# Optimization experiments

Hardware: AMD Instinct MI355X
Metric: run time of the kernel (lower is better)

## Reference

```python
import jax, jax.numpy as jnp
import numpy as np
from jax import lax

AGG_HOPS = 3
RANK_K = 10
NEG = -1e9


def _aggregate(embs, agg_w, agg_b, W_last, b_last):
    # GIKT-style multi-hop mean aggregation: embs[j] has shape [B, n1..nj, D]
    embs = list(embs)
    for i in range(AGG_HOPS):
        for j in range(AGG_HOPS - i):
            s = jnp.mean(embs[j + 1], axis=-2) + embs[j]
            embs[j] = jnp.tanh(s @ agg_w[j].T + agg_b[j])
    return jnp.tanh(embs[0] @ W_last.T + b_last)


def _hops(nodes0, tabA, tabB):
    # alternating bipartite neighbor expansion: [B] -> [B,n] -> [B,n,n] -> ...
    lst = [nodes0]
    for i in range(AGG_HOPS):
        tab = tabA if i % 2 == 0 else tabB
        lst.append(tab[lst[-1]])
    return lst


def _forward(user, question, response, mask, q_neighbors, s_neighbors, u_neighbors,
             q_neighbors_2, qs_index, emb_question, emb_question_2, emb_skill,
             emb_user, emb_response, w1_q, w2_q, W_ih, W_hh, b_ih, b_hh,
             agg_w, agg_b, W_agg_last, b_agg_last, W_query, b_query, W_key, b_key,
             W_w, b_w, W_fusion, b_fusion):
    B, T = question.shape
    D = emb_question.shape[1]
    emb_q_all = emb_question[question]  # [B,T,D], used for recap similarity
    wA, wB = W_w[0, :D], W_w[0, D:]     # MLP_W(cat(Q,K)) = Q@wA + K@wB + b

    def predict(qs_concat, states, svalid):
        ql = (qs_concat @ W_query.T + b_query) @ wA          # [B,Lq]
        kl = (states @ W_key.T + b_key) @ wB                 # [B,Ls]
        logit = ql[:, :, None] + kl[:, None, :] + b_w[0]     # [B,Lq,Ls]
        logit = jnp.where(svalid[:, None, :], logit, NEG)
        Lq, Ls = logit.shape[1], logit.shape[2]
        alpha = jax.nn.softmax(logit.reshape(B, -1), axis=1).reshape(B, Lq, Ls)
        g = jnp.einsum('bqd,bsd->bqs', qs_concat, states)
        return jax.nn.sigmoid(jnp.sum(alpha * g, axis=(1, 2)))

    def step(carry, t):
        h, c, sh = carry
        q_t, u_t, r_t = question[:, t], user[:, t], response[:, t]
        m = (mask[:, t] == 1)[:, None]  # [B,1]
        # question-skill GNN branch
        embs_q = [(emb_question if i % 2 == 0 else emb_skill)[n]
                  for i, n in enumerate(_hops(q_t, q_neighbors, s_neighbors))]
        e1 = jnp.where(m, _aggregate(embs_q, agg_w, agg_b, W_agg_last, b_agg_last),
                       emb_question[q_t])
        # user-question GNN branch
        embs_u = [(emb_user if i % 2 == 0 else emb_question_2)[n]
                  for i, n in enumerate(_hops(u_t, u_neighbors, q_neighbors_2))]
        e2 = jnp.where(m, _aggregate(embs_u, agg_w, agg_b, W_agg_last, b_agg_last),
                       emb_question_2[q_t])
        e_hat = w1_q * e1 + w2_q * e2
        e_t = jax.nn.relu(jnp.concatenate([e_hat, emb_response[r_t]], axis=1)
                          @ W_fusion.T + b_fusion)
        # masked LSTMCell (torch gate order i,f,g,o); dropout in eval mode
        gates = e_t @ W_ih.T + b_ih + h @ W_hh.T + b_hh
        gi, gf, gg, go = jnp.split(gates, 4, axis=1)
        c2 = jax.nn.sigmoid(gf) * c + jax.nn.sigmoid(gi) * jnp.tanh(gg)
        h2 = jax.nn.sigmoid(go) * jnp.tanh(c2)
        h = jnp.where(m, h2, h)
        c = jnp.where(m, c2, c)
        sh = lax.dynamic_update_slice(sh, h[:, None, :], (0, t, 0))
        # next question + its related skills
        q_next = question[:, t + 1]
        emb_qn = emb_question[q_next]
        qs_concat = jnp.concatenate([emb_qn[:, None, :], emb_skill[qs_index[q_next]]], axis=1)
        # soft recap: top-k past states by (detached) question similarity
        scores = lax.stop_gradient(jnp.einsum('btd,bd->bt', emb_q_all, emb_qn))
        valid_t = jnp.arange(T) < t
        scores = jnp.where(valid_t[None, :], scores, NEG)
        _, idx = lax.top_k(scores, RANK_K)                    # [B,K]
        sel = jnp.take_along_axis(sh, idx[:, :, None], axis=1)  # [B,K,D]
        svalid = jnp.concatenate([jnp.ones((B, 1), bool), valid_t[idx]], axis=1)
        states = jnp.concatenate([h[:, None, :], sel], axis=1)  # [B,1+K,D]
        y = predict(qs_concat, states, svalid)
        return (h, c, sh), y

    h0 = jnp.zeros((B, D), jnp.float32)
    sh0 = jnp.zeros((B, T, D), jnp.float32)
    _, ys = lax.scan(step, (h0, h0, sh0), jnp.arange(T - 1))
    return jnp.concatenate([jnp.full((B, 1), 0.5, jnp.float32), ys.T], axis=1)


def setup_inputs() -> dict:
    B, T, D = 32, 50, 100
    NQ, NS, NU = 20000, 500, 10000
    NBR, SPQ = 6, 4
    key = jax.random.key(0)
    ks = iter(jax.random.split(key, 48))
    nrm = lambda shape, sc: jax.random.normal(next(ks), shape, jnp.float32) * sc
    ri = lambda shape, hi: jax.random.randint(next(ks), shape, 0, hi, jnp.int32)
    s = 1.0 / float(np.sqrt(D))
    return {
        'user': ri((B, T), NU), 'question': ri((B, T), NQ),
        'response': ri((B, T), 2), 'mask': ri((B, T), 2),
        'q_neighbors': ri((NQ, NBR), NS), 's_neighbors': ri((NS, NBR), NQ),
        'u_neighbors': ri((NU, NBR), NQ), 'q_neighbors_2': ri((NQ, NBR), NU),
        'qs_index': ri((NQ, SPQ), NS),
        'emb_question': nrm((NQ, D), 0.1), 'emb_question_2': nrm((NQ, D), 0.1),
        'emb_skill': nrm((NS, D), 0.1), 'emb_user': nrm((NU, D), 0.1),
        'emb_response': nrm((2, D), 0.1),
        'w1_q': jnp.float32(0.5), 'w2_q': jnp.float32(0.5),
        'W_ih': nrm((4 * D, D), s), 'W_hh': nrm((4 * D, D), s),
        'b_ih': jnp.zeros((4 * D,), jnp.float32), 'b_hh': jnp.zeros((4 * D,), jnp.float32),
        'agg_w': nrm((3, D, D), s), 'agg_b': jnp.zeros((3, D), jnp.float32),
        'W_agg_last': nrm((D, D), s), 'b_agg_last': jnp.zeros((D,), jnp.float32),
        'W_query': nrm((D, D), s), 'b_query': jnp.zeros((D,), jnp.float32),
        'W_key': nrm((D, D), s), 'b_key': jnp.zeros((D,), jnp.float32),
        'W_w': nrm((1, 2 * D), s), 'b_w': jnp.zeros((1,), jnp.float32),
        'W_fusion': nrm((D, 2 * D), s), 'b_fusion': jnp.zeros((D,), jnp.float32),
    }


def reference(user, question, response, mask, q_neighbors, s_neighbors, u_neighbors,
              q_neighbors_2, qs_index, emb_question, emb_question_2, emb_skill,
              emb_user, emb_response, w1_q, w2_q, W_ih, W_hh, b_ih, b_hh,
              agg_w, agg_b, W_agg_last, b_agg_last, W_query, b_query, W_key, b_key,
              W_w, b_w, W_fusion, b_fusion):
    return _forward(user, question, response, mask, q_neighbors, s_neighbors,
                    u_neighbors, q_neighbors_2, qs_index, emb_question,
                    emb_question_2, emb_skill, emb_user, emb_response, w1_q, w2_q,
                    W_ih, W_hh, b_ih, b_hh, agg_w, agg_b, W_agg_last, b_agg_last,
                    W_query, b_query, W_key, b_key, W_w, b_w, W_fusion, b_fusion)
```

## Files before the change

kernel.cpp:

```cpp
#include <hip/hip_runtime.h>
#include <hip/hip_bf16.h>

#define BSZ 32
#define TT 50
#define TS 49
#define PH 101

#define OFF_GPRE  0u
#define OFF_QL    627200u
#define OFF_IDX   639744u
#define OFF_NV    655424u
#define OFF_QSC   656992u
#define OFF_E1    1440992u
#define OFF_E2    1597792u

#define RLF(v,l) __uint_as_float(__builtin_amdgcn_readlane(__float_as_uint(v), (l)))

__device__ __forceinline__ float tanh_fast(float x) {
    float e = __expf(2.f * x);
    return 1.f - __fdividef(2.f, e + 1.f);
}
__device__ __forceinline__ float sigm_fast(float x) {
    return __fdividef(1.f, 1.f + __expf(-x));
}
__device__ __forceinline__ float dot4(float4 a, float4 b) {
    return a.x*b.x + a.y*b.y + a.z*b.z + a.w*b.w;
}

__global__ __launch_bounds__(256, 2) void kagg(
    const int* __restrict__ user, const int* __restrict__ question, const int* __restrict__ mask,
    const int* __restrict__ qnbr, const int* __restrict__ snbr,
    const int* __restrict__ unbr, const int* __restrict__ qnbr2,
    const float* __restrict__ embQ, const float* __restrict__ embQ2, const float* __restrict__ embS,
    const float* __restrict__ embU,
    const float* __restrict__ aggw, const float* __restrict__ aggb,
    const float* __restrict__ wlast, const float* __restrict__ blast,
    float* __restrict__ WS)
{
    int bid = blockIdx.x;
    int tid = threadIdx.x;

    int pair = bid >> 1, which = bid & 1;
    int b = pair / TS, t = pair - b*TS;
    int mm = mask[b*TT + t];
    float* outE = WS + (which ? OFF_E2 : OFF_E1) + (size_t)pair*100;

    if (mm != 1) {
        int q_t = question[b*TT + t];
        const float4* src = (const float4*)((which ? embQ2 : embQ) + (size_t)q_t*100);
        if (tid < 25) ((float4*)outE)[tid] = src[tid];
        return;
    }

    int root = which ? user[b*TT + t] : question[b*TT + t];
    const int*   tabA = which ? unbr  : qnbr;
    const int*   tabB = which ? qnbr2 : snbr;
    const float4* eE = (const float4*)(which ? embU  : embQ);
    const float4* eO = (const float4*)(which ? embQ2 : embS);

    __shared__ __align__(16) float b2in[36*108];
    __shared__ __align__(16) float x1[6*108];
    __shared__ float s2v1b[600];
    __shared__ float v1a[600];
    __shared__ __align__(16) float x0[104], v0a[104], v0b[104];
    __shared__ int n1[8], n2[36], n3[216];

    if (tid < 6) n1[tid] = tabA[root*6 + tid];
    __syncthreads();
    if (tid < 36) n2[tid] = tabB[n1[tid/6]*6 + (tid % 6)];
    __syncthreads();
    if (tid < 216) n3[tid] = tabA[n2[tid/6]*6 + (tid % 6)];
    __syncthreads();
    for (int i4 = tid; i4 < 900; i4 += 256) {
        int v = i4 / 25, j = i4 - v*25;
        float4 a = eE[(size_t)n2[v]*25 + j];
        float4 s = make_float4(0.f, 0.f, 0.f, 0.f);
        const int* p = n3 + v*6;
        #pragma unroll
        for (int c = 0; c < 6; ++c) {
            float4 o = eO[(size_t)p[c]*25 + j];
            s.x += o.x; s.y += o.y; s.z += o.z; s.w += o.w;
        }
        float4 r = make_float4(a.x + s.x*(1.f/6.f), a.y + s.y*(1.f/6.f),
                               a.z + s.z*(1.f/6.f), a.w + s.w*(1.f/6.f));
        *(float4*)(b2in + v*108 + 4*j) = r;
    }
    for (int i4 = tid; i4 < 150; i4 += 256) {
        int a = i4 / 25, j = i4 - a*25;
        float4 base = eO[(size_t)n1[a]*25 + j];
        float4 s = make_float4(0.f, 0.f, 0.f, 0.f);
        #pragma unroll
        for (int c = 0; c < 6; ++c) {
            float4 o = eE[(size_t)n2[a*6 + c]*25 + j];
            s.x += o.x; s.y += o.y; s.z += o.z; s.w += o.w;
        }
        float4 r = make_float4(base.x + s.x*(1.f/6.f), base.y + s.y*(1.f/6.f),
                               base.z + s.z*(1.f/6.f), base.w + s.w*(1.f/6.f));
        *(float4*)(x1 + a*108 + 4*j) = r;
    }
    if (tid >= 160 && tid < 185) {
        int j = tid - 160;
        float4 base = eE[(size_t)root*25 + j];
        float4 s = make_float4(0.f, 0.f, 0.f, 0.f);
        #pragma unroll
        for (int a = 0; a < 6; ++a) {
            float4 o = eO[(size_t)n1[a]*25 + j];
            s.x += o.x; s.y += o.y; s.z += o.z; s.w += o.w;
        }
        float4 r = make_float4(base.x + s.x*(1.f/6.f), base.y + s.y*(1.f/6.f),
                               base.z + s.z*(1.f/6.f), base.w + s.w*(1.f/6.f));
        *(float4*)(x0 + 4*j) = r;
    }
    __syncthreads();
    if (tid < 150) {
        int dblk = tid / 6, a = tid - dblk*6, d0 = dblk*4;
        const float* wp = aggw + 20000 + d0*100;
        const float* xb = b2in + a*648;
        float acc[4][6];
        #pragma unroll
        for (int r = 0; r < 4; ++r)
            #pragma unroll
            for (int c = 0; c < 6; ++c) acc[r][c] = 0.f;
        #pragma unroll
        for (int j = 0; j < 25; ++j) {
            float4 r0 = *(const float4*)(wp + 4*j);
            float4 r1 = *(const float4*)(wp + 100 + 4*j);
            float4 r2 = *(const float4*)(wp + 200 + 4*j);
            float4 r3 = *(const float4*)(wp + 300 + 4*j);
            #pragma unroll
            for (int c = 0; c < 6; ++c) {
                float4 x = *(const float4*)(xb + c*108 + 4*j);
                acc[0][c] += dot4(r0, x);
                acc[1][c] += dot4(r1, x);
                acc[2][c] += dot4(r2, x);
                acc[3][c] += dot4(r3, x);
            }
        }
        #pragma unroll
        for (int r = 0; r < 4; ++r) {
            float bia = aggb[200 + d0 + r];
            float o = 0.f;
            #pragma unroll
            for (int c = 0; c < 6; ++c) o += tanh_fast(bia + acc[r][c]);
            s2v1b[a*100 + d0 + r] = o;
        }
    } else if (tid >= 160 && tid < 210) {
        int d0 = (tid - 160)*2;
        const float* wp = aggw + 10000 + d0*100;
        float a0[6], a1[6];
        #pragma unroll
        for (int c = 0; c < 6; ++c) { a0[c] = 0.f; a1[c] = 0.f; }
        #pragma unroll
        for (int j = 0; j < 25; ++j) {
            float4 r0 = *(const float4*)(wp + 4*j);
            float4 r1 = *(const float4*)(wp + 100 + 4*j);
            #pragma unroll
            for (int c = 0; c < 6; ++c) {
                float4 x = *(const float4*)(x1 + c*108 + 4*j);
                a0[c] += dot4(r0, x);
                a1[c] += dot4(r1, x);
            }
        }
        #pragma unroll
        for (int c = 0; c < 6; ++c) {
            v1a[c*100 + d0]     = tanh_fast(aggb[100 + d0] + a0[c]);
            v1a[c*100 + d0 + 1] = tanh_fast(aggb[100 + d0 + 1] + a1[c]);
        }
    } else if (tid >= 216 && tid < 241) {
        int d0 = (tid - 216)*4;
        const float* wp = aggw + d0*100;
        float a0 = 0.f, a1 = 0.f, a2 = 0.f, a3 = 0.f;
        #pragma unroll
        for (int j = 0; j < 25; ++j) {
            float4 x = *(const float4*)(x0 + 4*j);
            a0 += dot4(*(const float4*)(wp + 4*j), x);
            a1 += dot4(*(const float4*)(wp + 100 + 4*j), x);
            a2 += dot4(*(const float4*)(wp + 200 + 4*j), x);
            a3 += dot4(*(const float4*)(wp + 300 + 4*j), x);
        }
        v0a[d0]   = tanh_fast(aggb[d0] + a0);
        v0a[d0+1] = tanh_fast(aggb[d0+1] + a1);
        v0a[d0+2] = tanh_fast(aggb[d0+2] + a2);
        v0a[d0+3] = tanh_fast(aggb[d0+3] + a3);
    }
    __syncthreads();
    for (int e = tid; e < 600; e += 256) {
        int a = e / 100, d = e - a*100;
        x1[a*108 + d] = v1a[a*100 + d] + s2v1b[a*100 + d]*(1.f/6.f);
    }
    if (tid >= 128 && tid < 228) {
        int d = tid - 128;
        float s = 0.f;
        #pragma unroll
        for (int a = 0; a < 6; ++a) s += v1a[a*100 + d];
        x0[d] = v0a[d] + s*(1.f/6.f);
    }
    __syncthreads();
    if (tid < 50) {
        int d0 = tid*2;
        const float* wp = aggw + 10000 + d0*100;
        float a0[6], a1[6];
        #pragma unroll
        for (int c = 0; c < 6; ++c) { a0[c] = 0.f; a1[c] = 0.f; }
        #pragma unroll
        for (int j = 0; j < 25; ++j) {
            float4 r0 = *(const float4*)(wp + 4*j);
            float4 r1 = *(const float4*)(wp + 100 + 4*j);
            #pragma unroll
            for (int c = 0; c < 6; ++c) {
                float4 x = *(const float4*)(x1 + c*108 + 4*j);
                a0[c] += dot4(r0, x);
                a1[c] += dot4(r1, x);
            }
        }
        #pragma unroll
        for (int c = 0; c < 6; ++c) {
            s2v1b[c*100 + d0]     = tanh_fast(aggb[100 + d0] + a0[c]);
            s2v1b[c*100 + d0 + 1] = tanh_fast(aggb[100 + d0 + 1] + a1[c]);
        }
    } else if (tid >= 64 && tid < 89) {
        int d0 = (tid - 64)*4;
        const float* wp = aggw + d0*100;
        float a0 = 0.f, a1 = 0.f, a2 = 0.f, a3 = 0.f;
        #pragma unroll
        for (int j = 0; j < 25; ++j) {
            float4 x = *(const float4*)(x0 + 4*j);
            a0 += dot4(*(const float4*)(wp + 4*j), x);
            a1 += dot4(*(const float4*)(wp + 100 + 4*j), x);
            a2 += dot4(*(const float4*)(wp + 200 + 4*j), x);
            a3 += dot4(*(const float4*)(wp + 300 + 4*j), x);
        }
        v0b[d0]   = tanh_fast(aggb[d0] + a0);
        v0b[d0+1] = tanh_fast(aggb[d0+1] + a1);
        v0b[d0+2] = tanh_fast(aggb[d0+2] + a2);
        v0b[d0+3] = tanh_fast(aggb[d0+3] + a3);
    }
    __syncthreads();
    if (tid < 100) {
        float s = 0.f;
        #pragma unroll
        for (int a = 0; a < 6; ++a) s += s2v1b[a*100 + tid];
        x0[tid] = v0b[tid] + s*(1.f/6.f);
    }
    __syncthreads();
    if (tid < 25) {
        int d0 = tid*4;
        const float* wp = aggw + d0*100;
        float a0 = 0.f, a1 = 0.f, a2 = 0.f, a3 = 0.f;
        #pragma unroll
        for (int j = 0; j < 25; ++j) {
            float4 x = *(const float4*)(x0 + 4*j);
            a0 += dot4(*(const float4*)(wp + 4*j), x);
            a1 += dot4(*(const float4*)(wp + 100 + 4*j), x);
            a2 += dot4(*(const float4*)(wp + 200 + 4*j), x);
            a3 += dot4(*(const float4*)(wp + 300 + 4*j), x);
        }
        v0a[d0]   = tanh_fast(aggb[d0] + a0);
        v0a[d0+1] = tanh_fast(aggb[d0+1] + a1);
        v0a[d0+2] = tanh_fast(aggb[d0+2] + a2);
        v0a[d0+3] = tanh_fast(aggb[d0+3] + a3);
    }
    __syncthreads();
    if (tid < 25) {
        int d0 = tid*4;
        const float* wp = wlast + d0*100;
        float a0 = 0.f, a1 = 0.f, a2 = 0.f, a3 = 0.f;
        #pragma unroll
        for (int j = 0; j < 25; ++j) {
            float4 x = *(const float4*)(v0a + 4*j);
            a0 += dot4(*(const float4*)(wp + 4*j), x);
            a1 += dot4(*(const float4*)(wp + 100 + 4*j), x);
            a2 += dot4(*(const float4*)(wp + 200 + 4*j), x);
            a3 += dot4(*(const float4*)(wp + 300 + 4*j), x);
        }
        float4 r = make_float4(tanh_fast(blast[d0] + a0), tanh_fast(blast[d0+1] + a1),
                               tanh_fast(blast[d0+2] + a2), tanh_fast(blast[d0+3] + a3));
        *(float4*)(outE + d0) = r;
    }
}

__global__ __launch_bounds__(256, 2) void kfuse(
    const int* __restrict__ question, const int* __restrict__ response,
    const int* __restrict__ qsidx,
    const float* __restrict__ embQ, const float* __restrict__ embS, const float* __restrict__ embR,
    const float* __restrict__ w1p, const float* __restrict__ w2p,
    const float* __restrict__ wfus, const float* __restrict__ bfus,
    const float* __restrict__ wih, const float* __restrict__ bih, const float* __restrict__ bhh,
    const float* __restrict__ wq, const float* __restrict__ bq, const float* __restrict__ ww,
    float* __restrict__ WS)
{
    int bid = blockIdx.x;
    int b = bid / TS, t = bid - b*TS;
    int tid = threadIdx.x;
    size_t bt = (size_t)b*TS + t;

    __shared__ __align__(16) float sEIN[200], sET[112], sEQN[104], sQSCm[500];
    __shared__ float sWW[104], sVQ[104], sScore[52], sCq[1];

    int r_t = response[b*TT + t];
    int qn  = question[b*TT + t + 1];
    if (tid < 100) {
        sEIN[tid] = w1p[0]*WS[OFF_E1 + bt*100 + tid] + w2p[0]*WS[OFF_E2 + bt*100 + tid];
    } else if (tid < 200) {
        sEIN[tid] = embR[r_t*100 + (tid - 100)];
        if (tid < 150) {
            int d = tid - 100;
            sEQN[d]      = embQ[(size_t)qn*100 + d];
            sEQN[d + 50] = embQ[(size_t)qn*100 + d + 50];
        }
    } else {
        for (int i = tid - 200; i < 100; i += 56) sWW[i] = ww[i];
    }
    __syncthreads();
    if (tid < 160) {
        int slot = tid >> 4, k0 = tid & 15;
        #pragma unroll
        for (int rp = 0; rp < 10; ++rp) {
            int row = rp*10 + slot;
            const float* wr = wfus + row*200;
            float acc = 0.f;
            #pragma unroll
            for (int m = 0; m < 4; ++m) {
                int f4i = k0 + 16*m;
                if (f4i < 50)
                    acc += dot4(*(const float4*)(wr + 4*f4i), *(const float4*)(sEIN + 4*f4i));
            }
            acc += __shfl_xor(acc, 1); acc += __shfl_xor(acc, 2);
            acc += __shfl_xor(acc, 4); acc += __shfl_xor(acc, 8);
            if (k0 == 0) sET[row] = fmaxf(acc + bfus[row], 0.f);
        }
    } else {
        for (int k = tid - 160; k < 100; k += 96) {
            float a = 0.f;
            for (int d = 0; d < 100; ++d) a += sWW[d] * wq[d*100 + k];
            sVQ[k] = a;
        }
        if (tid == 255) {
            float a = 0.f;
            for (int d = 0; d < 100; ++d) a += bq[d] * sWW[d];
            sCq[0] = a;
        }
    }
    __syncthreads();
    {
        int slot = tid >> 4, k0 = tid & 15;
        #pragma unroll 4
        for (int rp = 0; rp < 25; ++rp) {
            int row = rp*16 + slot;
            const float* wr = wih + row*100;
            float acc = 0.f;
            #pragma unroll
            for (int m = 0; m < 2; ++m) {
                int f4i = k0 + 16*m;
                if (f4i < 25)
                    acc += dot4(*(const float4*)(wr + 4*f4i), *(const float4*)(sET + 4*f4i));
            }
            acc += __shfl_xor(acc, 1); acc += __shfl_xor(acc, 2);
            acc += __shfl_xor(acc, 4); acc += __shfl_xor(acc, 8);
            if (k0 == 0) WS[OFF_GPRE + bt*400 + row] = acc + bih[row] + bhh[row];
        }
    }
    if (tid < 125) {
        int q = tid / 25, j = tid - q*25;
        float4 val = (q == 0) ? *(const float4*)(sEQN + 4*j)
                              : ((const float4*)embS)[(size_t)qsidx[qn*4 + (q-1)]*25 + j];
        *(float4*)(sQSCm + q*100 + 4*j) = val;
        *(float4*)(WS + OFF_QSC + bt*500 + q*100 + 4*j) = val;
    } else if (tid >= 128 && tid < 128 + TS) {
        int tp = tid - 128;
        if (tp < t) {
            int qq = question[b*TT + tp];
            const float* er = embQ + (size_t)qq*100;
            float acc = 0.f;
            #pragma unroll
            for (int k = 0; k < 25; ++k)
                acc += dot4(*(const float4*)(er + 4*k), *(const float4*)(sEQN + 4*k));
            sScore[tp] = acc;
        }
    }
    __syncthreads();
    if (tid < 80) {
        int q = tid >> 4, kk = tid & 15;
        float acc = 0.f;
        #pragma unroll
        for (int j = 0; j < 7; ++j) {
            int k = kk + 16*j;
            if (k < 100) acc = fmaf(sQSCm[q*100 + k], sVQ[k], acc);
        }
        acc += __shfl_xor(acc, 1); acc += __shfl_xor(acc, 2);
        acc += __shfl_xor(acc, 4); acc += __shfl_xor(acc, 8);
        if (kk == 0) WS[OFF_QL + bt*8 + q] = acc + sCq[0];
    }
    if (tid >= 128 && tid < 192) {
        int lane = tid - 128;
        int nv = t < 10 ? t : 10;
        int* idxp = (int*)(WS + OFF_IDX) + bt*10;
        if (lane == 0) ((int*)(WS + OFF_NV))[bt] = nv;
        float v = (lane < t) ? sScore[lane] : -3.0e38f;
        int myidx = lane;
        int taken = 0;
        for (int p = 0; p < 10; ++p) {
            float vv = taken ? -3.0e38f : v;
            int ii = myidx;
            #pragma unroll
            for (int m = 1; m < 64; m <<= 1) {
                float v2 = __shfl_xor(vv, m);
                int   i2 = __shfl_xor(ii, m);
                if (v2 > vv || (v2 == vv && i2 < ii)) { vv = v2; ii = i2; }
            }
            if (p < nv) {
                if (lane == 0) idxp[p] = ii;
                if (myidx == ii) taken = 1;
            } else if (lane == 0) idxp[p] = 0;
        }
    }
}

__global__ __launch_bounds__(576) void kseq(
    const int* __restrict__ mask, const float* __restrict__ whh,
    const float* __restrict__ wk, const float* __restrict__ bk,
    const float* __restrict__ ww, const float* __restrict__ bwp,
    const float* __restrict__ WS, float* __restrict__ out)
{
    int b = blockIdx.x, tid = threadIdx.x, lane = tid & 63;
    __shared__ float sQSCall[TS*500];
    __shared__ float sSH[TS*PH + 3];
    __shared__ float sQLall[TS*8];
    __shared__ int   sIdxAll[TS*10];
    __shared__ int   sNvAll[TS];
    __shared__ int   sMask[TT];
    __shared__ float sH[104], sC[104], sG[400], sVKl[104];
    __shared__ float sKL2[2][12], sGv2[2][64];
    __shared__ float sCk[1];

    size_t b0 = (size_t)b*TS;
    int g = tid - 64;
    bool isGate = (g >= 0 && g < 400);

    float4 wv[25];
    if (isGate) {
        #pragma unroll
        for (int j = 0; j < 25; ++j) wv[j] = *(const float4*)(whh + g*100 + 4*j);
    }
    float gpre = isGate ? WS[OFF_GPRE + b0*400 + g] : 0.f;

    for (int i = tid; i < TS*500; i += 576) sQSCall[i] = WS[OFF_QSC + b0*500 + i];
    for (int i = tid; i < TS*8;   i += 576) sQLall[i]  = WS[OFF_QL + b0*8 + i];
    for (int i = tid; i < TS*10;  i += 576) sIdxAll[i] = ((const int*)(WS + OFF_IDX))[b0*10 + i];
    for (int i = tid; i < TS;     i += 576) sNvAll[i]  = ((const int*)(WS + OFF_NV))[b0 + i];
    if (tid < TT) sMask[tid] = mask[b*TT + tid];
    if (tid < 104) { sH[tid] = 0.f; sC[tid] = 0.f; }
    if (tid >= 104 && tid < 204) {
        int k = tid - 104;
        float a = 0.f;
        for (int d = 0; d < 100; ++d) a += ww[100 + d] * wk[d*100 + k];
        sVKl[k] = a;
    }
    if (tid == 204) {
        float a = 0.f;
        for (int d = 0; d < 100; ++d) a += bk[d] * ww[100 + d];
        sCk[0] = a;
    }
    if (tid == 205) out[b*TT] = 0.5f;
    float bw = bwp[0];
    __syncthreads();
    float ck = sCk[0];

    for (int t = 0; t < TS; ++t) {
        int par = t & 1;
        if (isGate) {
            float hA = sH[lane];
            float hB = sH[64 + (lane % 36)];
            float gpre_nx = 0.f;
            if (t + 1 < TS) gpre_nx = WS[OFF_GPRE + (b0 + t + 1)*400 + g];
            float a0 = 0.f, a1 = 0.f, a2 = 0.f, a3 = 0.f;
            #pragma unroll
            for (int j = 0; j < 25; ++j) {
                const int kb = 4*j;
                float h0, h1, h2, h3;
                if (kb < 64) {
                    h0 = RLF(hA, kb);   h1 = RLF(hA, kb+1);
                    h2 = RLF(hA, kb+2); h3 = RLF(hA, kb+3);
                } else {
                    h0 = RLF(hB, kb-64); h1 = RLF(hB, kb-63);
                    h2 = RLF(hB, kb-62); h3 = RLF(hB, kb-61);
                }
                a0 = fmaf(h0, wv[j].x, a0);
                a1 = fmaf(h1, wv[j].y, a1);
                a2 = fmaf(h2, wv[j].z, a2);
                a3 = fmaf(h3, wv[j].w, a3);
            }
            sG[g] = (a0 + a1) + (a2 + a3) + gpre;
            gpre = gpre_nx;
        } else if (tid >= 512) {
            int nv = sNvAll[t];
            if (lane < 60) {
                bool isKL = lane < 10;
                int s = isKL ? (lane + 1) : (((lane - 10) % 10) + 1);
                int q = isKL ? 0 : ((lane - 10) / 10);
                if (s <= nv) {
                    const float* st = sSH + sIdxAll[t*10 + s - 1]*PH;
                    const float* xp = isKL ? sVKl : (sQSCall + t*500 + q*100);
                    float c0 = 0.f, c1 = 0.f, c2 = 0.f, c3 = 0.f;
                    #pragma unroll
                    for (int k = 0; k < 100; k += 4) {
                        c0 = fmaf(st[k],   xp[k],   c0);
                        c1 = fmaf(st[k+1], xp[k+1], c1);
                        c2 = fmaf(st[k+2], xp[k+2], c2);
                        c3 = fmaf(st[k+3], xp[k+3], c3);
                    }
                    float acc = (c0 + c1) + (c2 + c3);
                    if (isKL) sKL2[par][s] = acc + ck;
                    else      sGv2[par][q*12 + s] = acc;
                }
            }
        } else if (tid < 64 && t > 0) {
            int tau = t - 1, par2 = tau & 1;
            int nv = sNvAll[tau];
            int dd = lane >> 3, k0 = lane & 7;
            if (dd < 6) {
                const float* xp = (dd == 0) ? sVKl : (sQSCall + tau*500 + (dd-1)*100);
                float acc = 0.f;
                #pragma unroll
                for (int jj = 0; jj < 13; ++jj) {
                    int k = k0 + 8*jj;
                    if (k < 100) acc = fmaf(sH[k], xp[k], acc);
                }
                acc += __shfl_xor(acc, 1); acc += __shfl_xor(acc, 2); acc += __shfl_xor(acc, 4);
                if (k0 == 0) {
                    if (dd == 0) sKL2[par2][0] = acc + ck;
                    else         sGv2[par2][(dd-1)*12] = acc;
                }
            }
            int q = lane / 11, s = lane - q*11;
            bool valid = (lane < 55) && (s <= nv);
            float lg = valid ? (sQLall[tau*8 + q] + sKL2[par2][s] + bw) : 0.f;
            float e  = valid ? __expf(lg) : 0.f;
            float gv = valid ? sGv2[par2][q*12 + s] : 0.f;
            float se = e, sg = e*gv;
            #pragma unroll
            for (int m = 1; m < 64; m <<= 1) { se += __shfl_xor(se, m); sg += __shfl_xor(sg, m); }
            if (lane == 0) out[b*TT + tau + 1] = __fdividef(1.f, 1.f + __expf(-__fdividef(sg, se)));
        }
        __syncthreads();
        if (g >= 0 && g < 100) {
            float gi = sG[g], gf = sG[100+g], gg = sG[200+g], go = sG[300+g];
            float c2 = sigm_fast(gf)*sC[g] + sigm_fast(gi)*tanh_fast(gg);
            float h2 = sigm_fast(go)*tanh_fast(c2);
            if (sMask[t] == 1) { sH[g] = h2; sC[g] = c2; }
            sSH[t*PH + g] = sH[g];
        }
        __syncthreads();
    }
    if (tid < 64) {
        int tau = TS - 1, par2 = tau & 1;
        int nv = sNvAll[tau];
        int dd = lane >> 3, k0 = lane & 7;
        if (dd < 6) {
            const float* xp = (dd == 0) ? sVKl : (sQSCall + tau*500 + (dd-1)*100);
            float acc = 0.f;
            #pragma unroll
            for (int jj = 0; jj < 13; ++jj) {
                int k = k0 + 8*jj;
                if (k < 100) acc = fmaf(sH[k], xp[k], acc);
            }
            acc += __shfl_xor(acc, 1); acc += __shfl_xor(acc, 2); acc += __shfl_xor(acc, 4);
            if (k0 == 0) {
                if (dd == 0) sKL2[par2][0] = acc + ck;
                else         sGv2[par2][(dd-1)*12] = acc;
            }
        }
        int q = lane / 11, s = lane - q*11;
        bool valid = (lane < 55) && (s <= nv);
        float lg = valid ? (sQLall[tau*8 + q] + sKL2[par2][s] + bw) : 0.f;
        float e  = valid ? __expf(lg) : 0.f;
        float gv = valid ? sGv2[par2][q*12 + s] : 0.f;
        float se = e, sg = e*gv;
        #pragma unroll
        for (int m = 1; m < 64; m <<= 1) { se += __shfl_xor(se, m); sg += __shfl_xor(sg, m); }
        if (lane == 0) out[b*TT + tau + 1] = __fdividef(1.f, 1.f + __expf(-__fdividef(sg, se)));
    }
}

extern "C" void kernel_launch(void* const* d_in, const int* in_sizes, int n_in,
                              void* d_out, int out_size, void* d_ws, size_t ws_size,
                              hipStream_t stream) {
    const int* user      = (const int*)d_in[0];
    const int* question  = (const int*)d_in[1];
    const int* response  = (const int*)d_in[2];
    const int* mask      = (const int*)d_in[3];
    const int* qnbr      = (const int*)d_in[4];
    const int* snbr      = (const int*)d_in[5];
    const int* unbr      = (const int*)d_in[6];
    const int* qnbr2     = (const int*)d_in[7];
    const int* qsidx     = (const int*)d_in[8];
    const float* embQ    = (const float*)d_in[9];
    const float* embQ2   = (const float*)d_in[10];
    const float* embS    = (const float*)d_in[11];
    const float* embU    = (const float*)d_in[12];
    const float* embR    = (const float*)d_in[13];
    const float* w1      = (const float*)d_in[14];
    const float* w2      = (const float*)d_in[15];
    const float* wih     = (const float*)d_in[16];
    const float* whh     = (const float*)d_in[17];
    const float* bih     = (const float*)d_in[18];
    const float* bhh     = (const float*)d_in[19];
    const float* aggw    = (const float*)d_in[20];
    const float* aggb    = (const float*)d_in[21];
    const float* wlast   = (const float*)d_in[22];
    const float* blast   = (const float*)d_in[23];
    const float* wq      = (const float*)d_in[24];
    const float* bq      = (const float*)d_in[25];
    const float* wk      = (const float*)d_in[26];
    const float* bk      = (const float*)d_in[27];
    const float* ww      = (const float*)d_in[28];
    const float* bwp     = (const float*)d_in[29];
    const float* wfus    = (const float*)d_in[30];
    const float* bfus    = (const float*)d_in[31];
    float* WS = (float*)d_ws;
    float* out = (float*)d_out;

    hipLaunchKernelGGL(kagg, dim3(2*BSZ*TS), dim3(256), 0, stream,
                       user, question, mask, qnbr, snbr, unbr, qnbr2,
                       embQ, embQ2, embS, embU, aggw, aggb, wlast, blast, WS);
    hipLaunchKernelGGL(kfuse, dim3(BSZ*TS), dim3(256), 0, stream,
                       question, response, qsidx, embQ, embS, embR,
                       w1, w2, wfus, bfus, wih, bih, bhh, wq, bq, ww, WS);
    hipLaunchKernelGGL(kseq, dim3(BSZ), dim3(576), 0, stream,
                       mask, whh, wk, bk, ww, bwp, WS, out);
}
```

Before: 414.6 us.

## Fuse aggregation and fusion kernels into one 512-thread block per step

Merges the two GNN-aggregation blocks (question and user side) and the fusion/gate-precompute kernel into a single kernel, with 512 threads per (b,t): each 256-thread half runs one aggregation side into shared memory, then all threads do the fusion stage. The E1/E2 workspace round trip and one kernel launch go away, and the fusion work is spread over more threads. kseq's shared-memory loads are also switched to float4. In exchange, per-block shared memory and thread count grow, which may lower occupancy, and the masked steps leave half the block idle.

```diff
diff --git a/kernel.cpp b/kernel.cpp
--- a/kernel.cpp
+++ b/kernel.cpp
@@ -11,8 +11,6 @@
 #define OFF_IDX   639744u
 #define OFF_NV    655424u
 #define OFF_QSC   656992u
-#define OFF_E1    1440992u
-#define OFF_E2    1597792u
 
 #define RLF(v,l) __uint_as_float(__builtin_amdgcn_readlane(__float_as_uint(v), (l)))
 
@@ -27,262 +25,17 @@
     return a.x*b.x + a.y*b.y + a.z*b.z + a.w*b.w;
 }
 
-__global__ __launch_bounds__(256, 2) void kagg(
-    const int* __restrict__ user, const int* __restrict__ question, const int* __restrict__ mask,
+__global__ __launch_bounds__(512) void kab(
+    const int* __restrict__ user, const int* __restrict__ question,
+    const int* __restrict__ response, const int* __restrict__ mask,
     const int* __restrict__ qnbr, const int* __restrict__ snbr,
     const int* __restrict__ unbr, const int* __restrict__ qnbr2,
-    const float* __restrict__ embQ, const float* __restrict__ embQ2, const float* __restrict__ embS,
-    const float* __restrict__ embU,
+    const int* __restrict__ qsidx,
+    const float* __restrict__ embQ, const float* __restrict__ embQ2,
+    const float* __restrict__ embS, const float* __restrict__ embU,
+    const float* __restrict__ embR,
     const float* __restrict__ aggw, const float* __restrict__ aggb,
     const float* __restrict__ wlast, const float* __restrict__ blast,
-    float* __restrict__ WS)
-{
-    int bid = blockIdx.x;
-    int tid = threadIdx.x;
-
-    int pair = bid >> 1, which = bid & 1;
-    int b = pair / TS, t = pair - b*TS;
-    int mm = mask[b*TT + t];
-    float* outE = WS + (which ? OFF_E2 : OFF_E1) + (size_t)pair*100;
-
-    if (mm != 1) {
-        int q_t = question[b*TT + t];
-        const float4* src = (const float4*)((which ? embQ2 : embQ) + (size_t)q_t*100);
-        if (tid < 25) ((float4*)outE)[tid] = src[tid];
-        return;
-    }
-
-    int root = which ? user[b*TT + t] : question[b*TT + t];
-    const int*   tabA = which ? unbr  : qnbr;
-    const int*   tabB = which ? qnbr2 : snbr;
-    const float4* eE = (const float4*)(which ? embU  : embQ);
-    const float4* eO = (const float4*)(which ? embQ2 : embS);
-
-    __shared__ __align__(16) float b2in[36*108];
-    __shared__ __align__(16) float x1[6*108];
-    __shared__ float s2v1b[600];
-    __shared__ float v1a[600];
-    __shared__ __align__(16) float x0[104], v0a[104], v0b[104];
-    __shared__ int n1[8], n2[36], n3[216];
-
-    if (tid < 6) n1[tid] = tabA[root*6 + tid];
-    __syncthreads();
-    if (tid < 36) n2[tid] = tabB[n1[tid/6]*6 + (tid % 6)];
-    __syncthreads();
-    if (tid < 216) n3[tid] = tabA[n2[tid/6]*6 + (tid % 6)];
-    __syncthreads();
-    for (int i4 = tid; i4 < 900; i4 += 256) {
-        int v = i4 / 25, j = i4 - v*25;
-        float4 a = eE[(size_t)n2[v]*25 + j];
-        float4 s = make_float4(0.f, 0.f, 0.f, 0.f);
-        const int* p = n3 + v*6;
-        #pragma unroll
-        for (int c = 0; c < 6; ++c) {
-            float4 o = eO[(size_t)p[c]*25 + j];
-            s.x += o.x; s.y += o.y; s.z += o.z; s.w += o.w;
-        }
-        float4 r = make_float4(a.x + s.x*(1.f/6.f), a.y + s.y*(1.f/6.f),
-                               a.z + s.z*(1.f/6.f), a.w + s.w*(1.f/6.f));
-        *(float4*)(b2in + v*108 + 4*j) = r;
-    }
-    for (int i4 = tid; i4 < 150; i4 += 256) {
-        int a = i4 / 25, j = i4 - a*25;
-        float4 base = eO[(size_t)n1[a]*25 + j];
-        float4 s = make_float4(0.f, 0.f, 0.f, 0.f);
-        #pragma unroll
-        for (int c = 0; c < 6; ++c) {
-            float4 o = eE[(size_t)n2[a*6 + c]*25 + j];
-            s.x += o.x; s.y += o.y; s.z += o.z; s.w += o.w;
-        }
-        float4 r = make_float4(base.x + s.x*(1.f/6.f), base.y + s.y*(1.f/6.f),
-                               base.z + s.z*(1.f/6.f), base.w + s.w*(1.f/6.f));
-        *(float4*)(x1 + a*108 + 4*j) = r;
-    }
-    if (tid >= 160 && tid < 185) {
-        int j = tid - 160;
-        float4 base = eE[(size_t)root*25 + j];
-        float4 s = make_float4(0.f, 0.f, 0.f, 0.f);
-        #pragma unroll
-        for (int a = 0; a < 6; ++a) {
-            float4 o = eO[(size_t)n1[a]*25 + j];
-            s.x += o.x; s.y += o.y; s.z += o.z; s.w += o.w;
-        }
-        float4 r = make_float4(base.x + s.x*(1.f/6.f), base.y + s.y*(1.f/6.f),
-                               base.z + s.z*(1.f/6.f), base.w + s.w*(1.f/6.f));
-        *(float4*)(x0 + 4*j) = r;
-    }
-    __syncthreads();
-    if (tid < 150) {
-        int dblk = tid / 6, a = tid - dblk*6, d0 = dblk*4;
-        const float* wp = aggw + 20000 + d0*100;
-        const float* xb = b2in + a*648;
-        float acc[4][6];
-        #pragma unroll
-        for (int r = 0; r < 4; ++r)
-            #pragma unroll
-            for (int c = 0; c < 6; ++c) acc[r][c] = 0.f;
-        #pragma unroll
-        for (int j = 0; j < 25; ++j) {
-            float4 r0 = *(const float4*)(wp + 4*j);
-            float4 r1 = *(const float4*)(wp + 100 + 4*j);
-            float4 r2 = *(const float4*)(wp + 200 + 4*j);
-            float4 r3 = *(const float4*)(wp + 300 + 4*j);
-            #pragma unroll
-            for (int c = 0; c < 6; ++c) {
-                float4 x = *(const float4*)(xb + c*108 + 4*j);
-                acc[0][c] += dot4(r0, x);
-                acc[1][c] += dot4(r1, x);
-                acc[2][c] += dot4(r2, x);
-                acc[3][c] += dot4(r3, x);
-            }
-        }
-        #pragma unroll
-        for (int r = 0; r < 4; ++r) {
-            float bia = aggb[200 + d0 + r];
-            float o = 0.f;
-            #pragma unroll
-            for (int c = 0; c < 6; ++c) o += tanh_fast(bia + acc[r][c]);
-            s2v1b[a*100 + d0 + r] = o;
-        }
-    } else if (tid >= 160 && tid < 210) {
-        int d0 = (tid - 160)*2;
-        const float* wp = aggw + 10000 + d0*100;
-        float a0[6], a1[6];
-        #pragma unroll
-        for (int c = 0; c < 6; ++c) { a0[c] = 0.f; a1[c] = 0.f; }
-        #pragma unroll
-        for (int j = 0; j < 25; ++j) {
-            float4 r0 = *(const float4*)(wp + 4*j);
-            float4 r1 = *(const float4*)(wp + 100 + 4*j);
-            #pragma unroll
-            for (int c = 0; c < 6; ++c) {
-                float4 x = *(const float4*)(x1 + c*108 + 4*j);
-                a0[c] += dot4(r0, x);
-                a1[c] += dot4(r1, x);
-            }
-        }
-        #pragma unroll
-        for (int c = 0; c < 6; ++c) {
-            v1a[c*100 + d0]     = tanh_fast(aggb[100 + d0] + a0[c]);
-            v1a[c*100 + d0 + 1] = tanh_fast(aggb[100 + d0 + 1] + a1[c]);
-        }
-    } else if (tid >= 216 && tid < 241) {
-        int d0 = (tid - 216)*4;
-        const float* wp = aggw + d0*100;
-        float a0 = 0.f, a1 = 0.f, a2 = 0.f, a3 = 0.f;
-        #pragma unroll
-        for (int j = 0; j < 25; ++j) {
-            float4 x = *(const float4*)(x0 + 4*j);
-            a0 += dot4(*(const float4*)(wp + 4*j), x);
-            a1 += dot4(*(const float4*)(wp + 100 + 4*j), x);
-            a2 += dot4(*(const float4*)(wp + 200 + 4*j), x);
-            a3 += dot4(*(const float4*)(wp + 300 + 4*j), x);
-        }
-        v0a[d0]   = tanh_fast(aggb[d0] + a0);
-        v0a[d0+1] = tanh_fast(aggb[d0+1] + a1);
-        v0a[d0+2] = tanh_fast(aggb[d0+2] + a2);
-        v0a[d0+3] = tanh_fast(aggb[d0+3] + a3);
-    }
-    __syncthreads();
-    for (int e = tid; e < 600; e += 256) {
-        int a = e / 100, d = e - a*100;
-        x1[a*108 + d] = v1a[a*100 + d] + s2v1b[a*100 + d]*(1.f/6.f);
-    }
-    if (tid >= 128 && tid < 228) {
-        int d = tid - 128;
-        float s = 0.f;
-        #pragma unroll
-        for (int a = 0; a < 6; ++a) s += v1a[a*100 + d];
-        x0[d] = v0a[d] + s*(1.f/6.f);
-    }
-    __syncthreads();
-    if (tid < 50) {
-        int d0 = tid*2;
-        const float* wp = aggw + 10000 + d0*100;
-        float a0[6], a1[6];
-        #pragma unroll
-        for (int c = 0; c < 6; ++c) { a0[c] = 0.f; a1[c] = 0.f; }
-        #pragma unroll
-        for (int j = 0; j < 25; ++j) {
-            float4 r0 = *(const float4*)(wp + 4*j);
-            float4 r1 = *(const float4*)(wp + 100 + 4*j);
-            #pragma unroll
-            for (int c = 0; c < 6; ++c) {
-                float4 x = *(const float4*)(x1 + c*108 + 4*j);
-                a0[c] += dot4(r0, x);
-                a1[c] += dot4(r1, x);
-            }
-        }
-        #pragma unroll
-        for (int c = 0; c < 6; ++c) {
-            s2v1b[c*100 + d0]     = tanh_fast(aggb[100 + d0] + a0[c]);
-            s2v1b[c*100 + d0 + 1] = tanh_fast(aggb[100 + d0 + 1] + a1[c]);
-        }
-    } else if (tid >= 64 && tid < 89) {
-        int d0 = (tid - 64)*4;
-        const float* wp = aggw + d0*100;
-        float a0 = 0.f, a1 = 0.f, a2 = 0.f, a3 = 0.f;
-        #pragma unroll
-        for (int j = 0; j < 25; ++j) {
-            float4 x = *(const float4*)(x0 + 4*j);
-            a0 += dot4(*(const float4*)(wp + 4*j), x);
-            a1 += dot4(*(const float4*)(wp + 100 + 4*j), x);
-            a2 += dot4(*(const float4*)(wp + 200 + 4*j), x);
-            a3 += dot4(*(const float4*)(wp + 300 + 4*j), x);
-        }
-        v0b[d0]   = tanh_fast(aggb[d0] + a0);
-        v0b[d0+1] = tanh_fast(aggb[d0+1] + a1);
-        v0b[d0+2] = tanh_fast(aggb[d0+2] + a2);
-        v0b[d0+3] = tanh_fast(aggb[d0+3] + a3);
-    }
-    __syncthreads();
-    if (tid < 100) {
-        float s = 0.f;
-        #pragma unroll
-        for (int a = 0; a < 6; ++a) s += s2v1b[a*100 + tid];
-        x0[tid] = v0b[tid] + s*(1.f/6.f);
-    }
-    __syncthreads();
-    if (tid < 25) {
-        int d0 = tid*4;
-        const float* wp = aggw + d0*100;
-        float a0 = 0.f, a1 = 0.f, a2 = 0.f, a3 = 0.f;
-        #pragma unroll
-        for (int j = 0; j < 25; ++j) {
-            float4 x = *(const float4*)(x0 + 4*j);
-            a0 += dot4(*(const float4*)(wp + 4*j), x);
-            a1 += dot4(*(const float4*)(wp + 100 + 4*j), x);
-            a2 += dot4(*(const float4*)(wp + 200 + 4*j), x);
-            a3 += dot4(*(const float4*)(wp + 300 + 4*j), x);
-        }
-        v0a[d0]   = tanh_fast(aggb[d0] + a0);
-        v0a[d0+1] = tanh_fast(aggb[d0+1] + a1);
-        v0a[d0+2] = tanh_fast(aggb[d0+2] + a2);
-        v0a[d0+3] = tanh_fast(aggb[d0+3] + a3);
-    }
-    __syncthreads();
-    if (tid < 25) {
-        int d0 = tid*4;
-        const float* wp = wlast + d0*100;
-        float a0 = 0.f, a1 = 0.f, a2 = 0.f, a3 = 0.f;
-        #pragma unroll
-        for (int j = 0; j < 25; ++j) {
-            float4 x = *(const float4*)(v0a + 4*j);
-            a0 += dot4(*(const float4*)(wp + 4*j), x);
-            a1 += dot4(*(const float4*)(wp + 100 + 4*j), x);
-            a2 += dot4(*(const float4*)(wp + 200 + 4*j), x);
-            a3 += dot4(*(const float4*)(wp + 300 + 4*j), x);
-        }
-        float4 r = make_float4(tanh_fast(blast[d0] + a0), tanh_fast(blast[d0+1] + a1),
-                               tanh_fast(blast[d0+2] + a2), tanh_fast(blast[d0+3] + a3));
-        *(float4*)(outE + d0) = r;
-    }
-}
-
-__global__ __launch_bounds__(256, 2) void kfuse(
-    const int* __restrict__ question, const int* __restrict__ response,
-    const int* __restrict__ qsidx,
-    const float* __restrict__ embQ, const float* __restrict__ embS, const float* __restrict__ embR,
     const float* __restrict__ w1p, const float* __restrict__ w2p,
     const float* __restrict__ wfus, const float* __restrict__ bfus,
     const float* __restrict__ wih, const float* __restrict__ bih, const float* __restrict__ bhh,
@@ -292,24 +45,271 @@
     int bid = blockIdx.x;
     int b = bid / TS, t = bid - b*TS;
     int tid = threadIdx.x;
+    int side = tid >> 8, ltid = tid & 255;
     size_t bt = (size_t)b*TS + t;
 
+    __shared__ __align__(16) float POOL[2][6608];
+    __shared__ int nbuf[2][264];
+    __shared__ __align__(16) float sE1[104], sE2[104];
     __shared__ __align__(16) float sEIN[200], sET[112], sEQN[104], sQSCm[500];
     __shared__ float sWW[104], sVQ[104], sScore[52], sCq[1];
 
+    int mm  = mask[b*TT + t];
+    int q_t = question[b*TT + t];
     int r_t = response[b*TT + t];
     int qn  = question[b*TT + t + 1];
+
+    if (mm == 1) {
+        int root = side ? user[b*TT + t] : q_t;
+        const int*    tabA = side ? unbr  : qnbr;
+        const int*    tabB = side ? qnbr2 : snbr;
+        const float4* eE   = (const float4*)(side ? embU  : embQ);
+        const float4* eO   = (const float4*)(side ? embQ2 : embS);
+        float* P     = POOL[side];
+        float* b2in  = P;
+        float* x1    = P + 3888;
+        float* s2v1b = P + 4536;
+        float* v1a   = P + 5136;
+        float* x0    = P + 5736;
+        float* v0a   = P + 5840;
+        float* v0b   = P + 5944;
+        int* n1 = nbuf[side];
+        int* n2 = n1 + 8;
+        int* n3 = n1 + 48;
+        float* sEout = side ? sE2 : sE1;
+
+        if (ltid < 6) n1[ltid] = tabA[root*6 + ltid];
+        __syncthreads();
+        if (ltid < 36) n2[ltid] = tabB[n1[ltid/6]*6 + (ltid % 6)];
+        __syncthreads();
+        if (ltid < 216) n3[ltid] = tabA[n2[ltid/6]*6 + (ltid % 6)];
+        __syncthreads();
+        for (int i4 = ltid; i4 < 900; i4 += 256) {
+            int v = i4 / 25, j = i4 - v*25;
+            float4 a = eE[(size_t)n2[v]*25 + j];
+            float4 s = make_float4(0.f, 0.f, 0.f, 0.f);
+            const int* p = n3 + v*6;
+            #pragma unroll
+            for (int c = 0; c < 6; ++c) {
+                float4 o = eO[(size_t)p[c]*25 + j];
+                s.x += o.x; s.y += o.y; s.z += o.z; s.w += o.w;
+            }
+            float4 r = make_float4(a.x + s.x*(1.f/6.f), a.y + s.y*(1.f/6.f),
+                                   a.z + s.z*(1.f/6.f), a.w + s.w*(1.f/6.f));
+            *(float4*)(b2in + v*108 + 4*j) = r;
+        }
+        for (int i4 = ltid; i4 < 150; i4 += 256) {
+            int a = i4 / 25, j = i4 - a*25;
+            float4 base = eO[(size_t)n1[a]*25 + j];
+            float4 s = make_float4(0.f, 0.f, 0.f, 0.f);
+            #pragma unroll
+            for (int c = 0; c < 6; ++c) {
+                float4 o = eE[(size_t)n2[a*6 + c]*25 + j];
+                s.x += o.x; s.y += o.y; s.z += o.z; s.w += o.w;
+            }
+            float4 r = make_float4(base.x + s.x*(1.f/6.f), base.y + s.y*(1.f/6.f),
+                                   base.z + s.z*(1.f/6.f), base.w + s.w*(1.f/6.f));
+            *(float4*)(x1 + a*108 + 4*j) = r;
+        }
+        if (ltid >= 160 && ltid < 185) {
+            int j = ltid - 160;
+            float4 base = eE[(size_t)root*25 + j];
+            float4 s = make_float4(0.f, 0.f, 0.f, 0.f);
+            #pragma unroll
+            for (int a = 0; a < 6; ++a) {
+                float4 o = eO[(size_t)n1[a]*25 + j];
+                s.x += o.x; s.y += o.y; s.z += o.z; s.w += o.w;
+            }
+            float4 r = make_float4(base.x + s.x*(1.f/6.f), base.y + s.y*(1.f/6.f),
+                                   base.z + s.z*(1.f/6.f), base.w + s.w*(1.f/6.f));
+            *(float4*)(x0 + 4*j) = r;
+        }
+        __syncthreads();
+        if (ltid < 150) {
+            int dblk = ltid / 6, a = ltid - dblk*6, d0 = dblk*4;
+            const float* wp = aggw + 20000 + d0*100;
+            const float* xb = b2in + a*648;
+            float acc[4][6];
+            #pragma unroll
+            for (int r = 0; r < 4; ++r)
+                #pragma unroll
+                for (int c = 0; c < 6; ++c) acc[r][c] = 0.f;
+            #pragma unroll
+            for (int j = 0; j < 25; ++j) {
+                float4 r0 = *(const float4*)(wp + 4*j);
+                float4 r1 = *(const float4*)(wp + 100 + 4*j);
+                float4 r2 = *(const float4*)(wp + 200 + 4*j);
+                float4 r3 = *(const float4*)(wp + 300 + 4*j);
+                #pragma unroll
+                for (int c = 0; c < 6; ++c) {
+                    float4 x = *(const float4*)(xb + c*108 + 4*j);
+                    acc[0][c] += dot4(r0, x);
+                    acc[1][c] += dot4(r1, x);
+                    acc[2][c] += dot4(r2, x);
+                    acc[3][c] += dot4(r3, x);
+                }
+            }
+            #pragma unroll
+            for (int r = 0; r < 4; ++r) {
+                float bia = aggb[200 + d0 + r];
+                float o = 0.f;
+                #pragma unroll
+                for (int c = 0; c < 6; ++c) o += tanh_fast(bia + acc[r][c]);
+                s2v1b[a*100 + d0 + r] = o;
+            }
+        } else if (ltid >= 160 && ltid < 210) {
+            int d0 = (ltid - 160)*2;
+            const float* wp = aggw + 10000 + d0*100;
+            float a0[6], a1[6];
+            #pragma unroll
+            for (int c = 0; c < 6; ++c) { a0[c] = 0.f; a1[c] = 0.f; }
+            #pragma unroll
+            for (int j = 0; j < 25; ++j) {
+                float4 r0 = *(const float4*)(wp + 4*j);
+                float4 r1 = *(const float4*)(wp + 100 + 4*j);
+                #pragma unroll
+                for (int c = 0; c < 6; ++c) {
+                    float4 x = *(const float4*)(x1 + c*108 + 4*j);
+                    a0[c] += dot4(r0, x);
+                    a1[c] += dot4(r1, x);
+                }
+            }
+            #pragma unroll
+            for (int c = 0; c < 6; ++c) {
+                v1a[c*100 + d0]     = tanh_fast(aggb[100 + d0] + a0[c]);
+                v1a[c*100 + d0 + 1] = tanh_fast(aggb[100 + d0 + 1] + a1[c]);
+            }
+        } else if (ltid >= 216 && ltid < 241) {
+            int d0 = (ltid - 216)*4;
+            const float* wp = aggw + d0*100;
+            float a0 = 0.f, a1 = 0.f, a2 = 0.f, a3 = 0.f;
+            #pragma unroll
+            for (int j = 0; j < 25; ++j) {
+                float4 x = *(const float4*)(x0 + 4*j);
+                a0 += dot4(*(const float4*)(wp + 4*j), x);
+                a1 += dot4(*(const float4*)(wp + 100 + 4*j), x);
+                a2 += dot4(*(const float4*)(wp + 200 + 4*j), x);
+                a3 += dot4(*(const float4*)(wp + 300 + 4*j), x);
+            }
+            v0a[d0]   = tanh_fast(aggb[d0] + a0);
+            v0a[d0+1] = tanh_fast(aggb[d0+1] + a1);
+            v0a[d0+2] = tanh_fast(aggb[d0+2] + a2);
+            v0a[d0+3] = tanh_fast(aggb[d0+3] + a3);
+        }
+        __syncthreads();
+        for (int e = ltid; e < 600; e += 256) {
+            int a = e / 100, d = e - a*100;
+            x1[a*108 + d] = v1a[a*100 + d] + s2v1b[a*100 + d]*(1.f/6.f);
+        }
+        if (ltid >= 128 && ltid < 228) {
+            int d = ltid - 128;
+            float s = 0.f;
+            #pragma unroll
+            for (int a = 0; a < 6; ++a) s += v1a[a*100 + d];
+            x0[d] = v0a[d] + s*(1.f/6.f);
+        }
+        __syncthreads();
+        if (ltid < 50) {
+            int d0 = ltid*2;
+            const float* wp = aggw + 10000 + d0*100;
+            float a0[6], a1[6];
+            #pragma unroll
+            for (int c = 0; c < 6; ++c) { a0[c] = 0.f; a1[c] = 0.f; }
+            #pragma unroll
+            for (int j = 0; j < 25; ++j) {
+                float4 r0 = *(const float4*)(wp + 4*j);
+                float4 r1 = *(const float4*)(wp + 100 + 4*j);
+                #pragma unroll
+                for (int c = 0; c < 6; ++c) {
+                    float4 x = *(const float4*)(x1 + c*108 + 4*j);
+                    a0[c] += dot4(r0, x);
+                    a1[c] += dot4(r1, x);
+                }
+            }
+            #pragma unroll
+            for (int c = 0; c < 6; ++c) {
+                s2v1b[c*100 + d0]     = tanh_fast(aggb[100 + d0] + a0[c]);
+                s2v1b[c*100 + d0 + 1] = tanh_fast(aggb[100 + d0 + 1] + a1[c]);
+            }
+        } else if (ltid >= 64 && ltid < 89) {
+            int d0 = (ltid - 64)*4;
+            const float* wp = aggw + d0*100;
+            float a0 = 0.f, a1 = 0.f, a2 = 0.f, a3 = 0.f;
+            #pragma unroll
+            for (int j = 0; j < 25; ++j) {
+                float4 x = *(const float4*)(x0 + 4*j);
+                a0 += dot4(*(const float4*)(wp + 4*j), x);
+                a1 += dot4(*(const float4*)(wp + 100 + 4*j), x);
+                a2 += dot4(*(const float4*)(wp + 200 + 4*j), x);
+                a3 += dot4(*(const float4*)(wp + 300 + 4*j), x);
+            }
+            v0b[d0]   = tanh_fast(aggb[d0] + a0);
+            v0b[d0+1] = tanh_fast(aggb[d0+1] + a1);
+            v0b[d0+2] = tanh_fast(aggb[d0+2] + a2);
+            v0b[d0+3] = tanh_fast(aggb[d0+3] + a3);
+        }
+        __syncthreads();
+        if (ltid < 100) {
+            float s = 0.f;
+            #pragma unroll
+            for (int a = 0; a < 6; ++a) s += s2v1b[a*100 + ltid];
+            x0[ltid] = v0b[ltid] + s*(1.f/6.f);
+        }
+        __syncthreads();
+        if (ltid < 25) {
+            int d0 = ltid*4;
+            const float* wp = aggw + d0*100;
+            float a0 = 0.f, a1 = 0.f, a2 = 0.f, a3 = 0.f;
+            #pragma unroll
+            for (int j = 0; j < 25; ++j) {
+                float4 x = *(const float4*)(x0 + 4*j);
+                a0 += dot4(*(const float4*)(wp + 4*j), x);
+                a1 += dot4(*(const float4*)(wp + 100 + 4*j), x);
+                a2 += dot4(*(const float4*)(wp + 200 + 4*j), x);
+                a3 += dot4(*(const float4*)(wp + 300 + 4*j), x);
+            }
+            v0a[d0]   = tanh_fast(aggb[d0] + a0);
+            v0a[d0+1] = tanh_fast(aggb[d0+1] + a1);
+            v0a[d0+2] = tanh_fast(aggb[d0+2] + a2);
+            v0a[d0+3] = tanh_fast(aggb[d0+3] + a3);
+        }
+        __syncthreads();
+        if (ltid < 25) {
+            int d0 = ltid*4;
+            const float* wp = wlast + d0*100;
+            float a0 = 0.f, a1 = 0.f, a2 = 0.f, a3 = 0.f;
+            #pragma unroll
+            for (int j = 0; j < 25; ++j) {
+                float4 x = *(const float4*)(v0a + 4*j);
+                a0 += dot4(*(const float4*)(wp + 4*j), x);
+                a1 += dot4(*(const float4*)(wp + 100 + 4*j), x);
+                a2 += dot4(*(const float4*)(wp + 200 + 4*j), x);
+                a3 += dot4(*(const float4*)(wp + 300 + 4*j), x);
+            }
+            float4 r = make_float4(tanh_fast(blast[d0] + a0), tanh_fast(blast[d0+1] + a1),
+                                   tanh_fast(blast[d0+2] + a2), tanh_fast(blast[d0+3] + a3));
+            *(float4*)(sEout + d0) = r;
+        }
+    } else {
+        if (tid < 25)
+            ((float4*)sE1)[tid] = ((const float4*)embQ)[(size_t)q_t*25 + tid];
+        else if (tid >= 256 && tid < 281)
+            ((float4*)sE2)[tid - 256] = ((const float4*)embQ2)[(size_t)q_t*25 + (tid - 256)];
+    }
+    __syncthreads();
+
     if (tid < 100) {
-        sEIN[tid] = w1p[0]*WS[OFF_E1 + bt*100 + tid] + w2p[0]*WS[OFF_E2 + bt*100 + tid];
+        sEIN[tid] = w1p[0]*sE1[tid] + w2p[0]*sE2[tid];
     } else if (tid < 200) {
         sEIN[tid] = embR[r_t*100 + (tid - 100)];
-        if (tid < 150) {
-            int d = tid - 100;
-            sEQN[d]      = embQ[(size_t)qn*100 + d];
-            sEQN[d + 50] = embQ[(size_t)qn*100 + d + 50];
-        }
-    } else {
-        for (int i = tid - 200; i < 100; i += 56) sWW[i] = ww[i];
+    } else if (tid < 300) {
+        sEQN[tid - 200] = embQ[(size_t)qn*100 + (tid - 200)];
+    } else if (tid < 400) {
+        sWW[tid - 300] = ww[tid - 300];
+    } else if (tid < 500) {
+        int i = tid - 400, q = i/25 + 1, j = i - (q-1)*25;
+        float4 v = ((const float4*)embS)[(size_t)qsidx[qn*4 + (q-1)]*25 + j];
+        *(float4*)(sQSCm + q*100 + 4*j) = v;
     }
     __syncthreads();
     if (tid < 160) {
@@ -329,7 +329,7 @@
             acc += __shfl_xor(acc, 4); acc += __shfl_xor(acc, 8);
             if (k0 == 0) sET[row] = fmaxf(acc + bfus[row], 0.f);
         }
-    } else {
+    } else if (tid < 256) {
         for (int k = tid - 160; k < 100; k += 96) {
             float a = 0.f;
             for (int d = 0; d < 100; ++d) a += sWW[d] * wq[d*100 + k];
@@ -340,34 +340,8 @@
             for (int d = 0; d < 100; ++d) a += bq[d] * sWW[d];
             sCq[0] = a;
         }
-    }
-    __syncthreads();
-    {
-        int slot = tid >> 4, k0 = tid & 15;
-        #pragma unroll 4
-        for (int rp = 0; rp < 25; ++rp) {
-            int row = rp*16 + slot;
-            const float* wr = wih + row*100;
-            float acc = 0.f;
-            #pragma unroll
-            for (int m = 0; m < 2; ++m) {
-                int f4i = k0 + 16*m;
-                if (f4i < 25)
-                    acc += dot4(*(const float4*)(wr + 4*f4i), *(const float4*)(sET + 4*f4i));
-            }
-            acc += __shfl_xor(acc, 1); acc += __shfl_xor(acc, 2);
-            acc += __shfl_xor(acc, 4); acc += __shfl_xor(acc, 8);
-            if (k0 == 0) WS[OFF_GPRE + bt*400 + row] = acc + bih[row] + bhh[row];
-        }
-    }
-    if (tid < 125) {
-        int q = tid / 25, j = tid - q*25;
-        float4 val = (q == 0) ? *(const float4*)(sEQN + 4*j)
-                              : ((const float4*)embS)[(size_t)qsidx[qn*4 + (q-1)]*25 + j];
-        *(float4*)(sQSCm + q*100 + 4*j) = val;
-        *(float4*)(WS + OFF_QSC + bt*500 + q*100 + 4*j) = val;
-    } else if (tid >= 128 && tid < 128 + TS) {
-        int tp = tid - 128;
+    } else if (tid < 256 + TS) {
+        int tp = tid - 256;
         if (tp < t) {
             int qq = question[b*TT + tp];
             const float* er = embQ + (size_t)qq*100;
@@ -377,10 +351,37 @@
                 acc += dot4(*(const float4*)(er + 4*k), *(const float4*)(sEQN + 4*k));
             sScore[tp] = acc;
         }
+    } else if (tid >= 320 && tid < 445) {
+        int i = tid - 320, q = i / 25, j = i - q*25;
+        float4 v = (q == 0) ? *(const float4*)(sEQN + 4*j)
+                            : *(const float4*)(sQSCm + q*100 + 4*j);
+        if (q == 0) *(float4*)(sQSCm + 4*j) = v;
+        *(float4*)(WS + OFF_QSC + bt*500 + q*100 + 4*j) = v;
     }
     __syncthreads();
-    if (tid < 80) {
-        int q = tid >> 4, kk = tid & 15;
+    {
+        int slot = tid >> 4, k0 = tid & 15;
+        #pragma unroll
+        for (int rp = 0; rp < 13; ++rp) {
+            int row = rp*32 + slot;
+            float acc = 0.f;
+            if (row < 400) {
+                const float* wr = wih + row*100;
+                #pragma unroll
+                for (int m = 0; m < 2; ++m) {
+                    int f4i = k0 + 16*m;
+                    if (f4i < 25)
+                        acc += dot4(*(const float4*)(wr + 4*f4i), *(const float4*)(sET + 4*f4i));
+                }
+            }
+            acc += __shfl_xor(acc, 1); acc += __shfl_xor(acc, 2);
+            acc += __shfl_xor(acc, 4); acc += __shfl_xor(acc, 8);
+            if (k0 == 0 && row < 400)
+                WS[OFF_GPRE + bt*400 + row] = acc + bih[row] + bhh[row];
+        }
+    }
+    if (tid >= 384 && tid < 464) {
+        int q = (tid - 384) >> 4, kk = tid & 15;
         float acc = 0.f;
         #pragma unroll
         for (int j = 0; j < 7; ++j) {
@@ -391,8 +392,8 @@
         acc += __shfl_xor(acc, 4); acc += __shfl_xor(acc, 8);
         if (kk == 0) WS[OFF_QL + bt*8 + q] = acc + sCq[0];
     }
-    if (tid >= 128 && tid < 192) {
-        int lane = tid - 128;
+    if (tid >= 320 && tid < 384) {
+        int lane = tid - 320;
         int nv = t < 10 ? t : 10;
         int* idxp = (int*)(WS + OFF_IDX) + bt*10;
         if (lane == 0) ((int*)(WS + OFF_NV))[bt] = nv;
@@ -423,9 +424,9 @@
     const float* __restrict__ WS, float* __restrict__ out)
 {
     int b = blockIdx.x, tid = threadIdx.x, lane = tid & 63;
-    __shared__ float sQSCall[TS*500];
+    __shared__ __align__(16) float sQSCall[TS*500];
     __shared__ float sSH[TS*PH + 3];
-    __shared__ float sQLall[TS*8];
+    __shared__ __align__(16) float sQLall[TS*8];
     __shared__ int   sIdxAll[TS*10];
     __shared__ int   sNvAll[TS];
     __shared__ int   sMask[TT];
@@ -444,8 +445,12 @@
     }
     float gpre = isGate ? WS[OFF_GPRE + b0*400 + g] : 0.f;
 
-    for (int i = tid; i < TS*500; i += 576) sQSCall[i] = WS[OFF_QSC + b0*500 + i];
-    for (int i = tid; i < TS*8;   i += 576) sQLall[i]  = WS[OFF_QL + b0*8 + i];
+    {
+        const float4* src = (const float4*)(WS + OFF_QSC + b0*500);
+        for (int i4 = tid; i4 < 6125; i4 += 576) ((float4*)sQSCall)[i4] = src[i4];
+        const float4* srq = (const float4*)(WS + OFF_QL + b0*8);
+        for (int i4 = tid; i4 < 98; i4 += 576) ((float4*)sQLall)[i4] = srq[i4];
+    }
     for (int i = tid; i < TS*10;  i += 576) sIdxAll[i] = ((const int*)(WS + OFF_IDX))[b0*10 + i];
     for (int i = tid; i < TS;     i += 576) sNvAll[i]  = ((const int*)(WS + OFF_NV))[b0 + i];
     if (tid < TT) sMask[tid] = mask[b*TT + tid];
@@ -620,11 +625,10 @@
     float* WS = (float*)d_ws;
     float* out = (float*)d_out;
 
-    hipLaunchKernelGGL(kagg, dim3(2*BSZ*TS), dim3(256), 0, stream,
-                       user, question, mask, qnbr, snbr, unbr, qnbr2,
-                       embQ, embQ2, embS, embU, aggw, aggb, wlast, blast, WS);
-    hipLaunchKernelGGL(kfuse, dim3(BSZ*TS), dim3(256), 0, stream,
-                       question, response, qsidx, embQ, embS, embR,
+    hipLaunchKernelGGL(kab, dim3(BSZ*TS), dim3(512), 0, stream,
+                       user, question, response, mask, qnbr, snbr, unbr, qnbr2, qsidx,
+                       embQ, embQ2, embS, embU, embR,
+                       aggw, aggb, wlast, blast,
                        w1, w2, wfus, bfus, wih, bih, bhh, wq, bq, ww, WS);
     hipLaunchKernelGGL(kseq, dim3(BSZ), dim3(576), 0, stream,
                        mask, whh, wk, bk, ww, bwp, WS, out);
```

Result: slower. 479.6 us (+15.7%).
